# Kernel tuning notes

Measured on AMD Instinct MI355X. Metric: run time of the kernel, lower is better.

## Reference

```python
import jax, jax.numpy as jnp
import numpy as np

HIDDEN = 1536
N_EXPERTS = 8
TOP_K = 2
N_GROUP = 1
TOPK_GROUP = 1
SCALE = 1.0


def setup_inputs() -> dict:
    key = jax.random.key(0)
    k1, k2 = jax.random.split(key)
    hidden_states = jax.random.normal(k1, (4, 4096, HIDDEN), dtype=jnp.float32)
    weight = jax.random.normal(k2, (N_EXPERTS, HIDDEN), dtype=jnp.float32) * 0.02
    e_score_correction_bias = jnp.zeros((N_EXPERTS,), dtype=jnp.float32)
    return {"hidden_states": hidden_states, "weight": weight,
            "e_score_correction_bias": e_score_correction_bias}


def reference(hidden_states, weight, e_score_correction_bias):
    # flatten tokens: (B*S, H)
    hs = hidden_states.reshape(-1, HIDDEN).astype(jnp.float32)
    router_logits = hs @ weight.astype(jnp.float32).T          # (T, E)
    scores = jax.nn.sigmoid(router_logits)                      # (T, E)

    # --- grouped top-k index selection (no-grad path in original) ---
    scores_for_choice = scores + e_score_correction_bias[None, :]
    per_group = scores_for_choice.reshape(-1, N_GROUP, N_EXPERTS // N_GROUP)
    # group score = sum of top-2 expert scores within each group
    group_scores = jax.lax.top_k(per_group, 2)[0].sum(axis=-1)  # (T, n_group)
    group_idx = jax.lax.top_k(group_scores, TOPK_GROUP)[1]      # (T, topk_group)
    group_mask = jnp.sum(jax.nn.one_hot(group_idx, N_GROUP, dtype=scores.dtype), axis=1)  # (T, n_group)
    score_mask = jnp.broadcast_to(group_mask[:, :, None], per_group.shape).reshape(-1, N_EXPERTS)
    masked_scores = jnp.where(score_mask > 0, scores_for_choice, 0.0)
    topk_indices = jax.lax.top_k(masked_scores, TOP_K)[1]       # (T, top_k) int32

    # --- gather weights from raw scores and normalize ---
    topk_weights = jnp.take_along_axis(scores, topk_indices, axis=1)  # (T, top_k)
    topk_weights = topk_weights / (topk_weights.sum(axis=-1, keepdims=True) + 1e-20)
    topk_weights = topk_weights * SCALE
    return topk_indices, topk_weights
```

## Files before the change

kernel.cpp:

```cpp
#include <hip/hip_runtime.h>
#include <math.h>

#define HID 1536
#define NEXP 8
#define NF4 (HID / 4)
#define TOKS_PER_BLOCK 32

__global__ __launch_bounds__(256) void router_topk_kernel(
    const float* __restrict__ hs,
    const float* __restrict__ wgt,
    const float* __restrict__ bias,
    float* __restrict__ out,
    int T)
{
    __shared__ float4 wlds[NEXP * NF4];

    const int tid = threadIdx.x;

    const float4* wg4 = reinterpret_cast<const float4*>(wgt);
    #pragma unroll
    for (int i = 0; i < (NEXP * NF4) / 256; ++i)
        wlds[tid + i * 256] = wg4[tid + i * 256];
    __syncthreads();

    const int lane = tid & 63;
    const int wid  = tid >> 6;
    const int q    = lane & 15;
    const int tg   = lane >> 4;
    const int base = blockIdx.x * TOKS_PER_BLOCK + wid * 8;
    const int tA   = base + tg;
    const int tB   = base + tg + 4;

    const float4* rowA = reinterpret_cast<const float4*>(hs) + (size_t)tA * NF4;
    const float4* rowB = reinterpret_cast<const float4*>(hs) + (size_t)tB * NF4;

    float accA[NEXP], accB[NEXP];
    #pragma unroll
    for (int e = 0; e < NEXP; ++e) { accA[e] = 0.0f; accB[e] = 0.0f; }

    #pragma unroll
    for (int c = 0; c < 4; ++c) {
        float4 hA[6], hB[6];
        #pragma unroll
        for (int j = 0; j < 6; ++j) {
            hA[j] = rowA[(c * 6 + j) * 16 + q];
            hB[j] = rowB[(c * 6 + j) * 16 + q];
        }
        #pragma unroll
        for (int j = 0; j < 6; ++j) {
            #pragma unroll
            for (int e = 0; e < NEXP; ++e) {
                const float4 wv = wlds[e * NF4 + (c * 6 + j) * 16 + q];
                accA[e] = fmaf(hA[j].x, wv.x, accA[e]);
                accA[e] = fmaf(hA[j].y, wv.y, accA[e]);
                accA[e] = fmaf(hA[j].z, wv.z, accA[e]);
                accA[e] = fmaf(hA[j].w, wv.w, accA[e]);
                accB[e] = fmaf(hB[j].x, wv.x, accB[e]);
                accB[e] = fmaf(hB[j].y, wv.y, accB[e]);
                accB[e] = fmaf(hB[j].z, wv.z, accB[e]);
                accB[e] = fmaf(hB[j].w, wv.w, accB[e]);
            }
        }
    }

    #pragma unroll
    for (int m = 1; m <= 8; m <<= 1) {
        #pragma unroll
        for (int e = 0; e < NEXP; ++e) {
            accA[e] += __shfl_xor(accA[e], m, 64);
            accB[e] += __shfl_xor(accB[e], m, 64);
        }
    }

    float sA[NEXP], scA[NEXP], sB[NEXP], scB[NEXP];
    #pragma unroll
    for (int e = 0; e < NEXP; ++e) {
        const float be = bias[e];
        sA[e]  = 1.0f / (1.0f + expf(-accA[e]));
        scA[e] = sA[e] + be;
        sB[e]  = 1.0f / (1.0f + expf(-accB[e]));
        scB[e] = sB[e] + be;
    }

    int   a0 = 0;
    float av0 = scA[0], aw0 = sA[0];
    #pragma unroll
    for (int e = 1; e < NEXP; ++e)
        if (scA[e] > av0) { av0 = scA[e]; aw0 = sA[e]; a0 = e; }
    int   a1 = -1;
    float av1 = -3.4e38f, aw1 = 0.0f;
    #pragma unroll
    for (int e = 0; e < NEXP; ++e)
        if (e != a0 && scA[e] > av1) { av1 = scA[e]; aw1 = sA[e]; a1 = e; }
    const float ainv = 1.0f / (aw0 + aw1 + 1e-20f);

    int   b0 = 0;
    float bv0 = scB[0], bw0 = sB[0];
    #pragma unroll
    for (int e = 1; e < NEXP; ++e)
        if (scB[e] > bv0) { bv0 = scB[e]; bw0 = sB[e]; b0 = e; }
    int   b1 = -1;
    float bv1 = -3.4e38f, bw1 = 0.0f;
    #pragma unroll
    for (int e = 0; e < NEXP; ++e)
        if (e != b0 && scB[e] > bv1) { bv1 = scB[e]; bw1 = sB[e]; b1 = e; }
    const float binv = 1.0f / (bw0 + bw1 + 1e-20f);

    if (q < 2 && tA < T) {
        out[tA * 2 + q]         = (q == 0) ? (float)a0 : (float)a1;
        out[T * 2 + tA * 2 + q] = ((q == 0) ? aw0 : aw1) * ainv;
    }
    if (q >= 2 && q < 4 && tB < T) {
        const int p = q - 2;
        out[tB * 2 + p]         = (p == 0) ? (float)b0 : (float)b1;
        out[T * 2 + tB * 2 + p] = ((p == 0) ? bw0 : bw1) * binv;
    }
}

extern "C" void kernel_launch(void* const* d_in, const int* in_sizes, int n_in,
                              void* d_out, int out_size, void* d_ws, size_t ws_size,
                              hipStream_t stream)
{
    const float* hs   = (const float*)d_in[0];
    const float* wgt  = (const float*)d_in[1];
    const float* bias = (const float*)d_in[2];
    float* out = (float*)d_out;

    const int T = in_sizes[0] / HID;
    const int blocks = (T + TOKS_PER_BLOCK - 1) / TOKS_PER_BLOCK;
    router_topk_kernel<<<blocks, 256, 0, stream>>>(hs, wgt, bias, out, T);
}
```

Before: 150.8 us.

## Drop LDS weight staging, read weights from global/L2 with double-buffered row loads

Removes the per-block copy of the full 48KB gate weight matrix into LDS and the barrier that follows it. Weights are now read directly from global memory, where they should stay cached across blocks. Each token row is split across 32 lanes instead of 16, and blocks shrink to 16 tokens with a min-blocks launch bound so more blocks can be resident. Row loads are double-buffered so the next chunk is fetched while the current one is computed, at the cost of more cache traffic for the weight reads.

After: 155.5 us. +3.1%, slower.

```diff
diff --git a/kernel.cpp b/kernel.cpp
--- a/kernel.cpp
+++ b/kernel.cpp
@@ -4,67 +4,70 @@
 #define HID 1536
 #define NEXP 8
 #define NF4 (HID / 4)
-#define TOKS_PER_BLOCK 32
+#define TOKS_PER_BLOCK 16
 
-__global__ __launch_bounds__(256) void router_topk_kernel(
+__global__ __launch_bounds__(256, 4) void router_topk_kernel(
     const float* __restrict__ hs,
     const float* __restrict__ wgt,
     const float* __restrict__ bias,
     float* __restrict__ out,
     int T)
 {
-    __shared__ float4 wlds[NEXP * NF4];
-
-    const int tid = threadIdx.x;
-
-    const float4* wg4 = reinterpret_cast<const float4*>(wgt);
-    #pragma unroll
-    for (int i = 0; i < (NEXP * NF4) / 256; ++i)
-        wlds[tid + i * 256] = wg4[tid + i * 256];
-    __syncthreads();
-
+    const int tid  = threadIdx.x;
     const int lane = tid & 63;
     const int wid  = tid >> 6;
-    const int q    = lane & 15;
-    const int tg   = lane >> 4;
-    const int base = blockIdx.x * TOKS_PER_BLOCK + wid * 8;
+    const int q    = lane & 31;
+    const int tg   = lane >> 5;
+    const int base = blockIdx.x * TOKS_PER_BLOCK + wid * 4;
     const int tA   = base + tg;
-    const int tB   = base + tg + 4;
+    const int tB   = base + tg + 2;
 
     const float4* rowA = reinterpret_cast<const float4*>(hs) + (size_t)tA * NF4;
     const float4* rowB = reinterpret_cast<const float4*>(hs) + (size_t)tB * NF4;
+    const float4* w4   = reinterpret_cast<const float4*>(wgt);
 
     float accA[NEXP], accB[NEXP];
     #pragma unroll
     for (int e = 0; e < NEXP; ++e) { accA[e] = 0.0f; accB[e] = 0.0f; }
 
-    #pragma unroll
-    for (int c = 0; c < 4; ++c) {
-        float4 hA[6], hB[6];
-        #pragma unroll
-        for (int j = 0; j < 6; ++j) {
-            hA[j] = rowA[(c * 6 + j) * 16 + q];
-            hB[j] = rowB[(c * 6 + j) * 16 + q];
-        }
-        #pragma unroll
-        for (int j = 0; j < 6; ++j) {
-            #pragma unroll
-            for (int e = 0; e < NEXP; ++e) {
-                const float4 wv = wlds[e * NF4 + (c * 6 + j) * 16 + q];
-                accA[e] = fmaf(hA[j].x, wv.x, accA[e]);
-                accA[e] = fmaf(hA[j].y, wv.y, accA[e]);
-                accA[e] = fmaf(hA[j].z, wv.z, accA[e]);
-                accA[e] = fmaf(hA[j].w, wv.w, accA[e]);
-                accB[e] = fmaf(hB[j].x, wv.x, accB[e]);
-                accB[e] = fmaf(hB[j].y, wv.y, accB[e]);
-                accB[e] = fmaf(hB[j].z, wv.z, accB[e]);
-                accB[e] = fmaf(hB[j].w, wv.w, accB[e]);
-            }
-        }
+    float4 b0A[4], b0B[4], b1A[4], b1B[4];
+
+#define LOADC(BA, BB, KB)                                   \
+    _Pragma("unroll")                                       \
+    for (int j = 0; j < 4; ++j) {                           \
+        BA[j] = rowA[(KB + j) * 32 + q];                    \
+        BB[j] = rowB[(KB + j) * 32 + q];                    \
     }
 
+#define COMPC(BA, BB, KB)                                   \
+    _Pragma("unroll")                                       \
+    for (int j = 0; j < 4; ++j) {                           \
+        _Pragma("unroll")                                   \
+        for (int e = 0; e < NEXP; ++e) {                    \
+            const float4 wv = w4[e * NF4 + (KB + j) * 32 + q]; \
+            accA[e] = fmaf(BA[j].x, wv.x, accA[e]);         \
+            accA[e] = fmaf(BA[j].y, wv.y, accA[e]);         \
+            accA[e] = fmaf(BA[j].z, wv.z, accA[e]);         \
+            accA[e] = fmaf(BA[j].w, wv.w, accA[e]);         \
+            accB[e] = fmaf(BB[j].x, wv.x, accB[e]);         \
+            accB[e] = fmaf(BB[j].y, wv.y, accB[e]);         \
+            accB[e] = fmaf(BB[j].z, wv.z, accB[e]);         \
+            accB[e] = fmaf(BB[j].w, wv.w, accB[e]);         \
+        }                                                   \
+    }
+
+    LOADC(b0A, b0B, 0)
+    LOADC(b1A, b1B, 4)
+    COMPC(b0A, b0B, 0)
+    LOADC(b0A, b0B, 8)
+    COMPC(b1A, b1B, 4)
+    COMPC(b0A, b0B, 8)
+
+#undef LOADC
+#undef COMPC
+
     #pragma unroll
-    for (int m = 1; m <= 8; m <<= 1) {
+    for (int m = 1; m <= 16; m <<= 1) {
         #pragma unroll
         for (int e = 0; e < NEXP; ++e) {
             accA[e] += __shfl_xor(accA[e], m, 64);
@@ -106,14 +109,15 @@
         if (e != b0 && scB[e] > bv1) { bv1 = scB[e]; bw1 = sB[e]; b1 = e; }
     const float binv = 1.0f / (bw0 + bw1 + 1e-20f);
 
-    if (q < 2 && tA < T) {
-        out[tA * 2 + q]         = (q == 0) ? (float)a0 : (float)a1;
-        out[T * 2 + tA * 2 + q] = ((q == 0) ? aw0 : aw1) * ainv;
+    const int p = lane & 31;
+    if (p < 2 && tA < T) {
+        out[tA * 2 + p]         = (p == 0) ? (float)a0 : (float)a1;
+        out[T * 2 + tA * 2 + p] = ((p == 0) ? aw0 : aw1) * ainv;
     }
-    if (q >= 2 && q < 4 && tB < T) {
-        const int p = q - 2;
-        out[tB * 2 + p]         = (p == 0) ? (float)b0 : (float)b1;
-        out[T * 2 + tB * 2 + p] = ((p == 0) ? bw0 : bw1) * binv;
+    if (p >= 2 && p < 4 && tB < T) {
+        const int pp = p - 2;
+        out[tB * 2 + pp]         = (pp == 0) ? (float)b0 : (float)b1;
+        out[T * 2 + tB * 2 + pp] = ((pp == 0) ? bw0 : bw1) * binv;
     }
 }
 
```

## Spread each token pair across a full wavefront with smaller blocks

Applied to the files above, without the earlier changes.

Each wavefront now handles two tokens using all 64 lanes across the hidden dimension, instead of eight tokens split over 16-lane groups. All hidden-state loads are issued up front, and blocks cover 8 tokens instead of 32, giving four times as many blocks. The aim is more coalesced, latency-hiding loads and more parallelism. The costs are extra shuffle-reduction stages and four times more copies of the 48KB weight matrix into LDS, which roughly doubles the traffic going through L2 into LDS.

Result: no change. 149.9 us (-0.6%).

```diff
diff --git a/kernel.cpp b/kernel.cpp
--- a/kernel.cpp
+++ b/kernel.cpp
@@ -4,9 +4,11 @@
 #define HID 1536
 #define NEXP 8
 #define NF4 (HID / 4)
-#define TOKS_PER_BLOCK 32
+#define WAVES_PER_BLOCK 4
+#define BLOCK (WAVES_PER_BLOCK * 64)
+#define TOKS_PER_BLOCK (WAVES_PER_BLOCK * 2)
 
-__global__ __launch_bounds__(256) void router_topk_kernel(
+__global__ __launch_bounds__(BLOCK, 8) void router_topk_kernel(
     const float* __restrict__ hs,
     const float* __restrict__ wgt,
     const float* __restrict__ bias,
@@ -19,52 +21,53 @@
 
     const float4* wg4 = reinterpret_cast<const float4*>(wgt);
     #pragma unroll
-    for (int i = 0; i < (NEXP * NF4) / 256; ++i)
-        wlds[tid + i * 256] = wg4[tid + i * 256];
+    for (int i = 0; i < (NEXP * NF4) / BLOCK; ++i)
+        wlds[tid + i * BLOCK] = wg4[tid + i * BLOCK];
     __syncthreads();
 
     const int lane = tid & 63;
     const int wid  = tid >> 6;
-    const int q    = lane & 15;
-    const int tg   = lane >> 4;
-    const int base = blockIdx.x * TOKS_PER_BLOCK + wid * 8;
-    const int tA   = base + tg;
-    const int tB   = base + tg + 4;
+    const int t0   = blockIdx.x * TOKS_PER_BLOCK + wid * 2;
+    const int t1   = t0 + 1;
 
-    const float4* rowA = reinterpret_cast<const float4*>(hs) + (size_t)tA * NF4;
-    const float4* rowB = reinterpret_cast<const float4*>(hs) + (size_t)tB * NF4;
+    const float4* rowA = reinterpret_cast<const float4*>(hs) + (size_t)t0 * NF4;
+    const float4* rowB = reinterpret_cast<const float4*>(hs) + (size_t)t1 * NF4;
+
+    const float4 hA0 = rowA[0 * 64 + lane], hB0 = rowB[0 * 64 + lane];
+    const float4 hA1 = rowA[1 * 64 + lane], hB1 = rowB[1 * 64 + lane];
+    const float4 hA2 = rowA[2 * 64 + lane], hB2 = rowB[2 * 64 + lane];
+    const float4 hA3 = rowA[3 * 64 + lane], hB3 = rowB[3 * 64 + lane];
+    const float4 hA4 = rowA[4 * 64 + lane], hB4 = rowB[4 * 64 + lane];
+    const float4 hA5 = rowA[5 * 64 + lane], hB5 = rowB[5 * 64 + lane];
 
     float accA[NEXP], accB[NEXP];
     #pragma unroll
     for (int e = 0; e < NEXP; ++e) { accA[e] = 0.0f; accB[e] = 0.0f; }
 
-    #pragma unroll
-    for (int c = 0; c < 4; ++c) {
-        float4 hA[6], hB[6];
-        #pragma unroll
-        for (int j = 0; j < 6; ++j) {
-            hA[j] = rowA[(c * 6 + j) * 16 + q];
-            hB[j] = rowB[(c * 6 + j) * 16 + q];
-        }
-        #pragma unroll
-        for (int j = 0; j < 6; ++j) {
-            #pragma unroll
-            for (int e = 0; e < NEXP; ++e) {
-                const float4 wv = wlds[e * NF4 + (c * 6 + j) * 16 + q];
-                accA[e] = fmaf(hA[j].x, wv.x, accA[e]);
-                accA[e] = fmaf(hA[j].y, wv.y, accA[e]);
-                accA[e] = fmaf(hA[j].z, wv.z, accA[e]);
-                accA[e] = fmaf(hA[j].w, wv.w, accA[e]);
-                accB[e] = fmaf(hB[j].x, wv.x, accB[e]);
-                accB[e] = fmaf(hB[j].y, wv.y, accB[e]);
-                accB[e] = fmaf(hB[j].z, wv.z, accB[e]);
-                accB[e] = fmaf(hB[j].w, wv.w, accB[e]);
-            }
-        }
+#define STEP(J, HA, HB)                                         \
+    _Pragma("unroll")                                           \
+    for (int e = 0; e < NEXP; ++e) {                            \
+        const float4 wv = wlds[e * NF4 + (J) * 64 + lane];      \
+        accA[e] = fmaf(HA.x, wv.x, accA[e]);                    \
+        accA[e] = fmaf(HA.y, wv.y, accA[e]);                    \
+        accA[e] = fmaf(HA.z, wv.z, accA[e]);                    \
+        accA[e] = fmaf(HA.w, wv.w, accA[e]);                    \
+        accB[e] = fmaf(HB.x, wv.x, accB[e]);                    \
+        accB[e] = fmaf(HB.y, wv.y, accB[e]);                    \
+        accB[e] = fmaf(HB.z, wv.z, accB[e]);                    \
+        accB[e] = fmaf(HB.w, wv.w, accB[e]);                    \
     }
 
+    STEP(0, hA0, hB0)
+    STEP(1, hA1, hB1)
+    STEP(2, hA2, hB2)
+    STEP(3, hA3, hB3)
+    STEP(4, hA4, hB4)
+    STEP(5, hA5, hB5)
+#undef STEP
+
     #pragma unroll
-    for (int m = 1; m <= 8; m <<= 1) {
+    for (int m = 1; m <= 32; m <<= 1) {
         #pragma unroll
         for (int e = 0; e < NEXP; ++e) {
             accA[e] += __shfl_xor(accA[e], m, 64);
@@ -106,14 +109,14 @@
         if (e != b0 && scB[e] > bv1) { bv1 = scB[e]; bw1 = sB[e]; b1 = e; }
     const float binv = 1.0f / (bw0 + bw1 + 1e-20f);
 
-    if (q < 2 && tA < T) {
-        out[tA * 2 + q]         = (q == 0) ? (float)a0 : (float)a1;
-        out[T * 2 + tA * 2 + q] = ((q == 0) ? aw0 : aw1) * ainv;
+    if (lane < 2 && t0 < T) {
+        out[t0 * 2 + lane]         = (lane == 0) ? (float)a0 : (float)a1;
+        out[T * 2 + t0 * 2 + lane] = ((lane == 0) ? aw0 : aw1) * ainv;
     }
-    if (q >= 2 && q < 4 && tB < T) {
-        const int p = q - 2;
-        out[tB * 2 + p]         = (p == 0) ? (float)b0 : (float)b1;
-        out[T * 2 + tB * 2 + p] = ((p == 0) ? bw0 : bw1) * binv;
+    if (lane >= 2 && lane < 4 && t1 < T) {
+        const int p = lane - 2;
+        out[t1 * 2 + p]         = (p == 0) ? (float)b0 : (float)b1;
+        out[T * 2 + t1 * 2 + p] = ((p == 0) ? bw0 : bw1) * binv;
     }
 }
 
@@ -128,5 +131,5 @@
 
     const int T = in_sizes[0] / HID;
     const int blocks = (T + TOKS_PER_BLOCK - 1) / TOKS_PER_BLOCK;
-    router_topk_kernel<<<blocks, 256, 0, stream>>>(hs, wgt, bias, out, T);
+    router_topk_kernel<<<blocks, BLOCK, 0, stream>>>(hs, wgt, bias, out, T);
 }
```
